# Kernel optimization log

Hardware: AMD Instinct MI355X
Metric: run time of the kernel (lower is better)

## Reference

```python
import jax, jax.numpy as jnp
import numpy as np

N, D_IN, D_OUT, H, E = 8192, 1024, 1024, 1024, 8
EPS = 0.2
S_FACTOR = 5.0


def setup_inputs() -> dict:
    key = jax.random.key(0)
    k0, k1, k2, k3 = jax.random.split(key, 4)
    x = jax.random.normal(k0, (N, D_IN), jnp.float32)
    # selector Linear(nIn, E); weights scaled by sFactor as in SMoE.__init__
    Wsel = jax.random.normal(k1, (D_IN, E), jnp.float32) * (S_FACTOR / np.sqrt(D_IN))
    bsel = jnp.zeros((E,), jnp.float32)
    # stacked 2-layer MLP experts: Linear(D_IN,H) -> ReLU -> Linear(H,D_OUT)
    W1 = jax.random.normal(k2, (E, D_IN, H), jnp.float32) / np.sqrt(D_IN)
    b1 = jnp.zeros((E, H), jnp.float32)
    W2 = jax.random.normal(k3, (E, H, D_OUT), jnp.float32) / np.sqrt(H)
    b2 = jnp.zeros((E, D_OUT), jnp.float32)
    return {"x": x, "Wsel": Wsel, "bsel": bsel, "W1": W1, "b1": b1, "W2": W2, "b2": b2}


def _sparse_weights(weightMat):
    # sort experts per token, descending (torch.sort(..., 1, descending=True))
    order = jnp.argsort(-weightMat, axis=1)                # [N,E]
    topW = jnp.take_along_axis(weightMat, order, axis=1)
    cumW = jnp.cumsum(topW, axis=1)
    capped = jnp.minimum(cumW, 1.0 - EPS)
    sw_sorted = jax.nn.relu(capped - cumW + topW)          # sparse weights, sorted order
    # softCost (side-effect metric in the original; not returned by SMoE.forward)
    shifted = jnp.pad(sw_sorted[:, 1:], ((0, 0), (0, 1)))
    _soft_cost = jnp.sum(jnp.where(shifted > 0, 1.0, sw_sorted), axis=1)
    # faithful to torch.gather(sparse_weight, 1, index) in the source
    sw = jnp.take_along_axis(sw_sorted, order, axis=1)     # [N,E]
    return sw


def reference(x, Wsel, bsel, W1, b1, W2, b2):
    weightMat = jax.nn.softmax(x @ Wsel + bsel, axis=1)    # [N,E] selector
    sw = _sparse_weights(weightMat)                        # [N,E] sparse combine weights
    # dense (vectorized) expert dispatch: tokens with sw==0 contribute 0,
    # numerically identical to the gather/scatter_add loop in sparse_MoE
    h = jax.nn.relu(jnp.einsum('nd,edh->enh', x, W1) + b1[:, None, :])   # [E,N,H]
    y = jnp.einsum('enh,eho->eno', h, W2) + b2[:, None, :]               # [E,N,O]
    out = jnp.einsum('ne,eno->no', sw, y)                                # [N,O]
    return out
```

## Files before the change

### kernel.cpp

```cpp
#include <hip/hip_runtime.h>
#include <hip/hip_bf16.h>
#include <stdint.h>

#define N_TOK 8192
#define DIN   1024
#define DOUT  1024
#define HID   1024
#define NE    8
#define CAP   0.8f

typedef __attribute__((ext_vector_type(8))) short short8;
typedef __attribute__((ext_vector_type(4))) float floatx4;

__device__ __forceinline__ void async_load16(const void* g, void* l) {
  __builtin_amdgcn_global_load_lds(
      (const __attribute__((address_space(1))) void*)g,
      (__attribute__((address_space(3))) void*)l,
      16, 0, 0);
}

__device__ __forceinline__ unsigned short bf16_bits(float f) {
  return __builtin_bit_cast(unsigned short, __float2bfloat16(f));
}

__global__ __launch_bounds__(256) void selector_kernel(
    const float* __restrict__ x, const float* __restrict__ Wsel,
    const float* __restrict__ bsel,
    __hip_bfloat16* __restrict__ x_bf, float* __restrict__ sw,
    float4* __restrict__ out4)
{
  {
    const int base = blockIdx.x * 4096 + threadIdx.x;
    const float4 z4 = {0.f, 0.f, 0.f, 0.f};
#pragma unroll
    for (int r = 0; r < 16; r++) out4[base + r * 256] = z4;
  }

  const int lane = threadIdx.x & 63;
  const int wave = threadIdx.x >> 6;
  const int tok0 = blockIdx.x * 16 + wave * 4;
  const float* xr = x + (size_t)tok0 * DIN;
  const float4* W4 = (const float4*)Wsel;

  float acc[4][8];
#pragma unroll
  for (int m = 0; m < 4; m++)
#pragma unroll
    for (int e = 0; e < 8; e++) acc[m][e] = 0.f;

#pragma unroll
  for (int i = 0; i < 16; i++) {
    const int d = lane + i * 64;
    const float4 wlo = W4[d * 2];
    const float4 whi = W4[d * 2 + 1];
#pragma unroll
    for (int m = 0; m < 4; m++) {
      const float xv = xr[m * DIN + d];
      acc[m][0] += xv * wlo.x; acc[m][1] += xv * wlo.y;
      acc[m][2] += xv * wlo.z; acc[m][3] += xv * wlo.w;
      acc[m][4] += xv * whi.x; acc[m][5] += xv * whi.y;
      acc[m][6] += xv * whi.z; acc[m][7] += xv * whi.w;
    }
  }
#pragma unroll
  for (int off = 32; off >= 1; off >>= 1)
#pragma unroll
    for (int m = 0; m < 4; m++)
#pragma unroll
      for (int e = 0; e < 8; e++) acc[m][e] += __shfl_xor(acc[m][e], off);

  if (lane < 4) {
    const int n = tok0 + lane;
    float w[8];
    float mx = -1e30f;
#pragma unroll
    for (int e = 0; e < 8; e++) { w[e] = acc[lane][e] + bsel[e]; mx = fmaxf(mx, w[e]); }
    float s = 0.f;
#pragma unroll
    for (int e = 0; e < 8; e++) { w[e] = expf(w[e] - mx); s += w[e]; }
    const float inv = 1.f / s;
#pragma unroll
    for (int e = 0; e < 8; e++) w[e] *= inv;

    float wsrt[8]; int ord[8];
    for (int k = 0; k < 8; k++) {
      const float v = w[k];
      int j = k;
      while (j > 0 && wsrt[j - 1] < v) { wsrt[j] = wsrt[j - 1]; ord[j] = ord[j - 1]; j--; }
      wsrt[j] = v; ord[j] = k;
    }
    float cum = 0.f, sws[8];
    for (int k = 0; k < 8; k++) {
      cum += wsrt[k];
      const float capped = fminf(cum, CAP);
      sws[k] = fmaxf(capped - cum + wsrt[k], 0.f);
    }
    for (int j = 0; j < 8; j++) sw[(size_t)n * 8 + j] = sws[ord[j]];
  }

  const float4* xr4 = (const float4*)xr;
  ushort4* xb4 = (ushort4*)(x_bf + (size_t)tok0 * DIN);
#pragma unroll
  for (int m = 0; m < 4; m++)
#pragma unroll
    for (int i = 0; i < 4; i++) {
      const int d4 = lane + i * 64;
      const float4 xv = xr4[m * 256 + d4];
      ushort4 p;
      p.x = bf16_bits(xv.x);
      p.y = bf16_bits(xv.y);
      p.z = bf16_bits(xv.z);
      p.w = bf16_bits(xv.w);
      xb4[m * 256 + d4] = p;
    }
}

__global__ __launch_bounds__(1024) void compact_convert_kernel(
    const float* __restrict__ sw, int* __restrict__ idx, int* __restrict__ cnt,
    const float* __restrict__ W1, const float* __restrict__ W2,
    __hip_bfloat16* __restrict__ W1t, __hip_bfloat16* __restrict__ W2t)
{
  const int z = blockIdx.z;
  const int t = threadIdx.x;

  if (z == 16) {
    const int bid = blockIdx.x + 16 * blockIdx.y;
    if (bid >= 8) return;
    const int e = bid;
    const int lane = t & 63;
    const int wv = t >> 6;
    __shared__ int wave_base[16];
    __shared__ int chunk_total;
    int base = 0;
#pragma unroll
    for (int c = 0; c < 8; c++) {
      const int tok = c * 1024 + t;
      const bool act = sw[(size_t)tok * 8 + e] > 0.f;
      const unsigned long long m = __ballot(act);
      const int before = __popcll(m & ((1ull << lane) - 1ull));
      if (lane == 0) wave_base[wv] = __popcll(m);
      __syncthreads();
      if (t == 0) {
        int s = 0;
        for (int w = 0; w < 16; w++) { const int v = wave_base[w]; wave_base[w] = s; s += v; }
        chunk_total = s;
      }
      __syncthreads();
      if (act) idx[e * N_TOK + base + wave_base[wv] + before] = tok;
      base += chunk_total;
      __syncthreads();
    }
    if (t == 0) cnt[e] = base;
    return;
  }

  __shared__ unsigned short tile[64][65];
  const float* src = (z & 8) ? W2 : W1;
  __hip_bfloat16* dst = (z & 8) ? W2t : W1t;
  const int e = z & 7;
  src += (size_t)e * 1024 * 1024;
  unsigned short* dstu = (unsigned short*)dst + (size_t)e * 1024 * 1024;
  const int R = blockIdx.y * 64, C = blockIdx.x * 64;

  {
    const int row = t >> 4;
    const int col4 = t & 15;
    const float4 v = *(const float4*)(src + (size_t)(R + row) * 1024 + C + col4 * 4);
    tile[row][col4 * 4 + 0] = bf16_bits(v.x);
    tile[row][col4 * 4 + 1] = bf16_bits(v.y);
    tile[row][col4 * 4 + 2] = bf16_bits(v.z);
    tile[row][col4 * 4 + 3] = bf16_bits(v.w);
  }
  __syncthreads();
  {
    const int d = t >> 4;
    const int j = t & 15;
    ushort4 o;
    o.x = tile[j * 4 + 0][d];
    o.y = tile[j * 4 + 1][d];
    o.z = tile[j * 4 + 2][d];
    o.w = tile[j * 4 + 3][d];
    *(ushort4*)(dstu + (size_t)(C + d) * 1024 + R + j * 4) = o;
  }
}

#define BUFO (128 * 32)

template <int MODE>
__global__ __launch_bounds__(256, 2) void moe_gemm(
    const __hip_bfloat16* __restrict__ x_bf,
    __hip_bfloat16* __restrict__ hpool,
    const __hip_bfloat16* __restrict__ Wt,
    const float* __restrict__ biasAll,
    const float* __restrict__ sw,
    const int* __restrict__ idx, const int* __restrict__ cnt,
    float* __restrict__ out)
{
  const int e = blockIdx.z;
  const int count = cnt[e];
  const int m0 = blockIdx.y * 128;
  if (m0 >= count) return;
  const int n0 = blockIdx.x * 128;

  __shared__ __align__(16) __hip_bfloat16 sA[3 * BUFO];
  __shared__ __align__(16) __hip_bfloat16 sB[3 * BUFO];
  const int t = threadIdx.x;
  const int lane = t & 63;
  const int wave = t >> 6;
  const int wm = (wave & 1) * 64;
  const int wn = (wave >> 1) * 64;
  const int* idx_e = idx + e * N_TOK;
  const float* bias = biasAll + e * 1024;

  floatx4 acc[4][4];
#pragma unroll
  for (int i = 0; i < 4; i++)
#pragma unroll
    for (int j = 0; j < 4; j++) acc[i][j] = (floatx4){0.f, 0.f, 0.f, 0.f};

  const int sr = t >> 2;
  const int sc = (t & 3) * 8;
  const __hip_bfloat16* Ag0;
  const __hip_bfloat16* Ag1;
  if (MODE == 0) {
    const int t0 = idx_e[min(m0 + sr, count - 1)];
    const int t1 = idx_e[min(m0 + sr + 64, count - 1)];
    Ag0 = x_bf + (size_t)t0 * 1024 + sc;
    Ag1 = x_bf + (size_t)t1 * 1024 + sc;
  } else {
    const __hip_bfloat16* hp = hpool + (size_t)e * N_TOK * 1024;
    Ag0 = hp + (size_t)(m0 + sr) * 1024 + sc;
    Ag1 = hp + (size_t)(m0 + sr + 64) * 1024 + sc;
  }
  const __hip_bfloat16* Bg = Wt + (size_t)e * 1024 * 1024 + (size_t)(n0 + sr) * 1024 + sc;
  __hip_bfloat16* lA = &sA[sr * 32 + sc];
  __hip_bfloat16* lB = &sB[sr * 32 + sc];

  const int rf = lane & 15;
  const int k8 = (lane >> 4) * 8;
  const int roA = (wm + rf) * 32 + k8;
  const int roB = (wn + rf) * 32 + k8;

#define STAGE(KT, WB)                                                           \
  {                                                                             \
    const int kof = (KT) * 32;                                                  \
    async_load16(Ag0 + kof, lA + (WB) * BUFO);                                  \
    async_load16(Ag1 + kof, lA + (WB) * BUFO + 64 * 32);                        \
    async_load16(Bg + kof, lB + (WB) * BUFO);                                   \
    async_load16(Bg + (size_t)64 * 1024 + kof, lB + (WB) * BUFO + 64 * 32);     \
  }

#define P2ITER(KT, RB, WB, WAIT, DOSTAGE)                                       \
  {                                                                             \
    if (DOSTAGE) STAGE((KT) + 2, WB);                                           \
    asm volatile("s_waitcnt " WAIT ::: "memory");                               \
    const __hip_bfloat16* pA = &sA[(RB) * BUFO + roA];                          \
    const __hip_bfloat16* pB = &sB[(RB) * BUFO + roB];                          \
    short8 aF[4], bF[4];                                                        \
    _Pragma("unroll")                                                           \
    for (int i = 0; i < 4; i++) aF[i] = *(const short8*)(pA + i * 16 * 32);     \
    _Pragma("unroll")                                                           \
    for (int j = 0; j < 4; j++) bF[j] = *(const short8*)(pB + j * 16 * 32);     \
    __builtin_amdgcn_s_setprio(1);                                              \
    _Pragma("unroll")                                                           \
    for (int i = 0; i < 4; i++)                                                 \
      _Pragma("unroll")                                                         \
      for (int j = 0; j < 4; j++)                                               \
        acc[i][j] = __builtin_amdgcn_mfma_f32_16x16x32_bf16(aF[i], bF[j],       \
                                                            acc[i][j], 0, 0, 0);\
    __builtin_amdgcn_s_setprio(0);                                              \
    __builtin_amdgcn_s_barrier();                                               \
  }

  STAGE(0, 0);
  STAGE(1, 1);
  asm volatile("s_waitcnt vmcnt(4)" ::: "memory");
  __builtin_amdgcn_s_barrier();

#pragma unroll 1
  for (int kt = 0; kt < 30; kt += 3) {
    P2ITER(kt,     0, 2, "vmcnt(4)", true);
    P2ITER(kt + 1, 1, 0, "vmcnt(4)", true);
    P2ITER(kt + 2, 2, 1, "vmcnt(4)", true);
  }
  P2ITER(30, 0, 0, "vmcnt(0)", false);
  P2ITER(31, 1, 0, "vmcnt(0)", false);
#undef P2ITER
#undef STAGE

  const int quad = lane >> 4;
  const int cn = lane & 15;
#pragma unroll
  for (int i = 0; i < 4; i++) {
#pragma unroll
    for (int r = 0; r < 4; r++) {
      const int gm = m0 + wm + i * 16 + quad * 4 + r;
      if (gm >= count) continue;
      int tok = 0; float swv = 0.f;
      if (MODE == 1) {
        tok = idx_e[gm];
        swv = sw[tok * 8 + e];
      }
#pragma unroll
      for (int j = 0; j < 4; j++) {
        const int gn = n0 + wn + j * 16 + cn;
        const float v = acc[i][j][r] + bias[gn];
        if (MODE == 0) {
          hpool[((size_t)e * N_TOK + gm) * 1024 + gn] = __float2bfloat16(fmaxf(v, 0.f));
        } else {
          unsafeAtomicAdd(&out[(size_t)tok * 1024 + gn], swv * v);
        }
      }
    }
  }
}

extern "C" void kernel_launch(void* const* d_in, const int* in_sizes, int n_in,
                              void* d_out, int out_size, void* d_ws, size_t ws_size,
                              hipStream_t stream) {
  const float* x    = (const float*)d_in[0];
  const float* Wsel = (const float*)d_in[1];
  const float* bsel = (const float*)d_in[2];
  const float* W1   = (const float*)d_in[3];
  const float* b1   = (const float*)d_in[4];
  const float* W2   = (const float*)d_in[5];
  const float* b2   = (const float*)d_in[6];
  float* out = (float*)d_out;

  char* ws = (char*)d_ws;
  __hip_bfloat16* x_bf = (__hip_bfloat16*)ws; ws += (size_t)N_TOK * DIN * 2;
  __hip_bfloat16* W1t  = (__hip_bfloat16*)ws; ws += (size_t)NE * DIN * HID * 2;
  __hip_bfloat16* W2t  = (__hip_bfloat16*)ws; ws += (size_t)NE * HID * DOUT * 2;
  float* sw            = (float*)ws;          ws += (size_t)N_TOK * NE * 4;
  int* idx             = (int*)ws;            ws += (size_t)NE * N_TOK * 4;
  int* cnt             = (int*)ws;            ws += 256;
  __hip_bfloat16* hpool = (__hip_bfloat16*)ws;

  selector_kernel<<<N_TOK / 16, 256, 0, stream>>>(x, Wsel, bsel, x_bf, sw,
                                                  (float4*)out);
  compact_convert_kernel<<<dim3(16, 16, 17), 1024, 0, stream>>>(
      sw, idx, cnt, W1, W2, W1t, W2t);

  moe_gemm<0><<<dim3(HID / 128, N_TOK / 128, NE), 256, 0, stream>>>(
      x_bf, hpool, W1t, b1, sw, idx, cnt, out);
  moe_gemm<1><<<dim3(DOUT / 128, N_TOK / 128, NE), 256, 0, stream>>>(
      x_bf, hpool, W2t, b2, sw, idx, cnt, out);
}
```

Baseline: 319.7 us.

## Restructure MoE GEMM mainloop with K=64 tiles, XOR-swizzled LDS and phased staging

Replaces the triple-buffered K=32 pipeline with a double-buffered K=64 pipeline in a single 64KB LDS array. Rows are XOR-swizzled to avoid bank conflicts on fragment reads. Each k-tile is split into four barrier-separated phases, with A and B global->LDS loads staggered between them so memory traffic overlaps MFMA work. B fragments are held in registers across phases. This aims to cut LDS bank conflicts and barrier count per FLOP, but the 64KB LDS per block may limit occupancy against the 2-blocks launch bound.

```diff
diff --git a/kernel.cpp b/kernel.cpp
--- a/kernel.cpp
+++ b/kernel.cpp
@@ -184,8 +184,6 @@
   }
 }
 
-#define BUFO (128 * 32)
-
 template <int MODE>
 __global__ __launch_bounds__(256, 2) void moe_gemm(
     const __hip_bfloat16* __restrict__ x_bf,
@@ -202,8 +200,8 @@
   if (m0 >= count) return;
   const int n0 = blockIdx.x * 128;
 
-  __shared__ __align__(16) __hip_bfloat16 sA[3 * BUFO];
-  __shared__ __align__(16) __hip_bfloat16 sB[3 * BUFO];
+  __shared__ __align__(16) char lds[65536];
+
   const int t = threadIdx.x;
   const int lane = t & 63;
   const int wave = t >> 6;
@@ -218,75 +216,109 @@
 #pragma unroll
     for (int j = 0; j < 4; j++) acc[i][j] = (floatx4){0.f, 0.f, 0.f, 0.f};
 
-  const int sr = t >> 2;
-  const int sc = (t & 3) * 8;
-  const __hip_bfloat16* Ag0;
-  const __hip_bfloat16* Ag1;
-  if (MODE == 0) {
-    const int t0 = idx_e[min(m0 + sr, count - 1)];
-    const int t1 = idx_e[min(m0 + sr + 64, count - 1)];
-    Ag0 = x_bf + (size_t)t0 * 1024 + sc;
-    Ag1 = x_bf + (size_t)t1 * 1024 + sc;
-  } else {
-    const __hip_bfloat16* hp = hpool + (size_t)e * N_TOK * 1024;
-    Ag0 = hp + (size_t)(m0 + sr) * 1024 + sc;
-    Ag1 = hp + (size_t)(m0 + sr + 64) * 1024 + sc;
-  }
-  const __hip_bfloat16* Bg = Wt + (size_t)e * 1024 * 1024 + (size_t)(n0 + sr) * 1024 + sc;
-  __hip_bfloat16* lA = &sA[sr * 32 + sc];
-  __hip_bfloat16* lB = &sB[sr * 32 + sc];
-
-  const int rf = lane & 15;
-  const int k8 = (lane >> 4) * 8;
-  const int roA = (wm + rf) * 32 + k8;
-  const int roB = (wn + rf) * 32 + k8;
-
-#define STAGE(KT, WB)                                                           \
+  const int srow = t >> 3;
+  const int scol = ((t & 7) * 16) ^ ((srow & 7) << 4);
+  const char* aSrc[2][2];
+  const char* bSrc[2][2];
+  const __hip_bfloat16* hp = hpool + (size_t)e * N_TOK * 1024;
+#pragma unroll
+  for (int h = 0; h < 2; h++)
+#pragma unroll
+    for (int j = 0; j < 2; j++) {
+      const int rA = h * 64 + j * 32 + srow;
+      if (MODE == 0) {
+        const int tok = idx_e[min(m0 + rA, count - 1)];
+        aSrc[h][j] = (const char*)(x_bf + (size_t)tok * 1024) + scol;
+      } else {
+        aSrc[h][j] = (const char*)(hp + (size_t)(m0 + rA) * 1024) + scol;
+      }
+      bSrc[h][j] = (const char*)(Wt + (size_t)e * 1024 * 1024 +
+                                 (size_t)(n0 + rA) * 1024) + scol;
+    }
+
+  const int fr = lane & 15;
+  const int frx = (fr & 7) << 4;
+  const int q16 = (lane >> 4) << 4;
+  const int colk0 = (0 + q16) ^ frx;
+  const int colk1 = (64 + q16) ^ frx;
+  const int rowOff[4] = { (0 * 16 + fr) * 128, (1 * 16 + fr) * 128,
+                          (2 * 16 + fr) * 128, (3 * 16 + fr) * 128 };
+  const int aReg = (wave & 1) * 8192;
+  const int bReg = 32768 + (wave >> 1) * 8192;
+
+  short8 bF00, bF01, bF10, bF11, bF20, bF21, bF30, bF31;
+
+#define STAGE_A(KT, PAR, H)                                                     \
   {                                                                             \
-    const int kof = (KT) * 32;                                                  \
-    async_load16(Ag0 + kof, lA + (WB) * BUFO);                                  \
-    async_load16(Ag1 + kof, lA + (WB) * BUFO + 64 * 32);                        \
-    async_load16(Bg + kof, lB + (WB) * BUFO);                                   \
-    async_load16(Bg + (size_t)64 * 1024 + kof, lB + (WB) * BUFO + 64 * 32);     \
-  }
-
-#define P2ITER(KT, RB, WB, WAIT, DOSTAGE)                                       \
+    async_load16(aSrc[H][0] + (KT) * 128, lds + ((PAR)*2 + (H)) * 8192 + t*16); \
+    async_load16(aSrc[H][1] + (KT) * 128,                                       \
+                 lds + ((PAR)*2 + (H)) * 8192 + 4096 + t*16);                   \
+  }
+#define STAGE_B(KT, PAR, H)                                                     \
   {                                                                             \
-    if (DOSTAGE) STAGE((KT) + 2, WB);                                           \
-    asm volatile("s_waitcnt " WAIT ::: "memory");                               \
-    const __hip_bfloat16* pA = &sA[(RB) * BUFO + roA];                          \
-    const __hip_bfloat16* pB = &sB[(RB) * BUFO + roB];                          \
-    short8 aF[4], bF[4];                                                        \
-    _Pragma("unroll")                                                           \
-    for (int i = 0; i < 4; i++) aF[i] = *(const short8*)(pA + i * 16 * 32);     \
-    _Pragma("unroll")                                                           \
-    for (int j = 0; j < 4; j++) bF[j] = *(const short8*)(pB + j * 16 * 32);     \
+    async_load16(bSrc[H][0] + (KT) * 128,                                       \
+                 lds + 32768 + ((PAR)*2 + (H)) * 8192 + t*16);                  \
+    async_load16(bSrc[H][1] + (KT) * 128,                                       \
+                 lds + 32768 + ((PAR)*2 + (H)) * 8192 + 4096 + t*16);           \
+  }
+#define RA(P, I, CK) (*(const short8*)(lds + (P)*16384 + aReg + rowOff[I] + (CK)))
+#define RB(P, N, CK) (*(const short8*)(lds + (P)*16384 + bReg + rowOff[N] + (CK)))
+
+#define PHASEM(P, I)                                                            \
+  {                                                                             \
+    const short8 a0 = RA(P, I, colk0);                                          \
+    const short8 a1 = RA(P, I, colk1);                                          \
     __builtin_amdgcn_s_setprio(1);                                              \
-    _Pragma("unroll")                                                           \
-    for (int i = 0; i < 4; i++)                                                 \
-      _Pragma("unroll")                                                         \
-      for (int j = 0; j < 4; j++)                                               \
-        acc[i][j] = __builtin_amdgcn_mfma_f32_16x16x32_bf16(aF[i], bF[j],       \
-                                                            acc[i][j], 0, 0, 0);\
+    acc[I][0] = __builtin_amdgcn_mfma_f32_16x16x32_bf16(a0, bF00, acc[I][0], 0, 0, 0); \
+    acc[I][0] = __builtin_amdgcn_mfma_f32_16x16x32_bf16(a1, bF01, acc[I][0], 0, 0, 0); \
+    acc[I][1] = __builtin_amdgcn_mfma_f32_16x16x32_bf16(a0, bF10, acc[I][1], 0, 0, 0); \
+    acc[I][1] = __builtin_amdgcn_mfma_f32_16x16x32_bf16(a1, bF11, acc[I][1], 0, 0, 0); \
+    acc[I][2] = __builtin_amdgcn_mfma_f32_16x16x32_bf16(a0, bF20, acc[I][2], 0, 0, 0); \
+    acc[I][2] = __builtin_amdgcn_mfma_f32_16x16x32_bf16(a1, bF21, acc[I][2], 0, 0, 0); \
+    acc[I][3] = __builtin_amdgcn_mfma_f32_16x16x32_bf16(a0, bF30, acc[I][3], 0, 0, 0); \
+    acc[I][3] = __builtin_amdgcn_mfma_f32_16x16x32_bf16(a1, bF31, acc[I][3], 0, 0, 0); \
     __builtin_amdgcn_s_setprio(0);                                              \
+  }
+
+#define QUAD(KT, P, PN, WAITS, DOA, DOB)                                        \
+  {                                                                             \
+    asm volatile("s_waitcnt " WAITS ::: "memory");                              \
     __builtin_amdgcn_s_barrier();                                               \
-  }
-
-  STAGE(0, 0);
-  STAGE(1, 1);
-  asm volatile("s_waitcnt vmcnt(4)" ::: "memory");
-  __builtin_amdgcn_s_barrier();
+    if (DOA) STAGE_A((KT) + 1, PN, 0);                                          \
+    bF00 = RB(P, 0, colk0); bF01 = RB(P, 0, colk1);                             \
+    bF10 = RB(P, 1, colk0); bF11 = RB(P, 1, colk1);                             \
+    bF20 = RB(P, 2, colk0); bF21 = RB(P, 2, colk1);                             \
+    bF30 = RB(P, 3, colk0); bF31 = RB(P, 3, colk1);                             \
+    PHASEM(P, 0);                                                               \
+    __builtin_amdgcn_s_barrier();                                               \
+    if (DOA) STAGE_A((KT) + 1, PN, 1);                                          \
+    PHASEM(P, 1);                                                               \
+    __builtin_amdgcn_s_barrier();                                               \
+    if (DOB) STAGE_B((KT) + 2, P, 0);                                           \
+    PHASEM(P, 2);                                                               \
+    __builtin_amdgcn_s_barrier();                                               \
+    if (DOB) STAGE_B((KT) + 2, P, 1);                                           \
+    PHASEM(P, 3);                                                               \
+  }
+
+  STAGE_A(0, 0, 0); STAGE_A(0, 0, 1);
+  STAGE_B(0, 0, 0); STAGE_B(0, 0, 1);
+  STAGE_B(1, 1, 0); STAGE_B(1, 1, 1);
 
 #pragma unroll 1
-  for (int kt = 0; kt < 30; kt += 3) {
-    P2ITER(kt,     0, 2, "vmcnt(4)", true);
-    P2ITER(kt + 1, 1, 0, "vmcnt(4)", true);
-    P2ITER(kt + 2, 2, 1, "vmcnt(4)", true);
-  }
-  P2ITER(30, 0, 0, "vmcnt(0)", false);
-  P2ITER(31, 1, 0, "vmcnt(0)", false);
-#undef P2ITER
-#undef STAGE
+  for (int kt = 0; kt < 14; kt += 2) {
+    QUAD(kt,     0, 1, "vmcnt(4)", 1, 1);
+    QUAD(kt + 1, 1, 0, "vmcnt(4)", 1, 1);
+  }
+  QUAD(14, 0, 1, "vmcnt(4)", 1, 0);
+  QUAD(15, 1, 0, "vmcnt(0)", 0, 0);
+
+#undef QUAD
+#undef PHASEM
+#undef RB
+#undef RA
+#undef STAGE_B
+#undef STAGE_A
 
   const int quad = lane >> 4;
   const int cn = lane & 15;
```

Result: faster. 295.7 us (-7.5%).
